# Kernel tuning notes

Hardware: AMD Instinct MI355X
Metric: run time of the kernel (lower is better)

The kernel has to match this reference:

```python
import jax, jax.numpy as jnp
import numpy as np

B, C, H, W = 16, 128, 128, 128
CO = C // 2  # conv output channels


def _binary_activation(x):
    # forward: sign(x); backward: piecewise-polynomial surrogate (STE)
    out_fwd = jnp.sign(x)
    m1 = (x < -1).astype(x.dtype)
    m2 = (x < 0).astype(x.dtype)
    m3 = (x < 1).astype(x.dtype)
    out1 = -1.0 * m1 + (x * x + 2.0 * x) * (1.0 - m1)
    out2 = out1 * m2 + (-x * x + 2.0 * x) * (1.0 - m2)
    out3 = out2 * m3 + 1.0 * (1.0 - m3)
    return jax.lax.stop_gradient(out_fwd) - jax.lax.stop_gradient(out3) + out3


def _binary_weights(conv_w):
    w = conv_w.reshape(CO, C, 3, 3)
    # per-output-channel mean(|w|), detached
    sf = jax.lax.stop_gradient(jnp.mean(jnp.abs(w), axis=(1, 2, 3), keepdims=True))
    bw_ng = sf * jnp.sign(w)
    wc = jnp.clip(w, -1.0, 1.0)
    return jax.lax.stop_gradient(bw_ng) - jax.lax.stop_gradient(wc) + wc


def setup_inputs() -> dict:
    key = jax.random.key(0)
    k1, k2, k3 = jax.random.split(key, 3)
    x = jax.random.normal(k1, (B, C, H, W), dtype=jnp.float32)
    bias1 = jnp.zeros((1, C, 1, 1), dtype=jnp.float32)
    prelu_a = jnp.full((1, C, 1, 1), 0.25, dtype=jnp.float32)
    bias2 = jnp.zeros((1, C, 1, 1), dtype=jnp.float32)
    # stored flat like HardBinaryConv.weights; zero-mean so signs are mixed
    conv_w = jax.random.normal(k2, (CO * C * 9, 1), dtype=jnp.float32) * 0.001
    # grouped 1x1 conv: groups=CO, 2 input channels per group
    pool_w = jax.random.normal(k3, (CO, 2, 1, 1), dtype=jnp.float32) * 0.1
    return {"x": x, "bias1": bias1, "prelu_a": prelu_a, "bias2": bias2,
            "conv_w": conv_w, "pool_w": pool_w}


def reference(x, bias1, prelu_a, bias2, conv_w, pool_w):
    b, c, h, w = x.shape
    co = c // 2
    out = x + bias1
    out = jnp.maximum(out, 0.0) + prelu_a * jnp.minimum(out, 0.0)  # PReLU per-channel
    out = out + bias2
    out = _binary_activation(out)
    bw = _binary_weights(conv_w)
    y = jax.lax.conv_general_dilated(out, bw, window_strides=(1, 1),
                                     padding=((1, 1), (1, 1)),
                                     dimension_numbers=("NCHW", "OIHW", "NCHW"))
    # grouped 1x1 channel pool: out chan o = w[o,0]*x[2o] + w[o,1]*x[2o+1]
    shortcut = jnp.sum(x.reshape(b, co, 2, h, w) * pool_w.reshape(1, co, 2, 1, 1), axis=2)
    y = y + shortcut
    # PixelUnshuffle(2): (B,co,H,W) -> (B,4*co,H/2,W/2)
    ho, wo = h // 2, w // 2
    y = y.reshape(b, co, ho, 2, wo, 2).transpose(0, 1, 3, 5, 2, 4).reshape(b, co * 4, ho, wo)
    return y
```

## Files before the change

### kernel.cpp

```cpp
#include <hip/hip_runtime.h>
#include <stdint.h>

typedef __attribute__((ext_vector_type(4))) float f32x4;
typedef __attribute__((ext_vector_type(4))) unsigned int u32x4;
typedef __attribute__((ext_vector_type(2))) long long i64x2;
typedef long long i64_t;

#define NB 16
#define NC 128
#define NH 128
#define NW 128
#define WP 130

__device__ __forceinline__ int swz7(int wp) { return (wp ^ (wp >> 3)) & 7; }

__global__ __launch_bounds__(256) void k_prep(const float* __restrict__ cw,
                                              const float* __restrict__ b1,
                                              const float* __restrict__ pa,
                                              const float* __restrict__ b2,
                                              float* __restrict__ sf,
                                              float* __restrict__ theta,
                                              unsigned char* __restrict__ wf) {
    int b = blockIdx.x, t = threadIdx.x;
    int f = b * 256 + t;
    int j   = f & 7;
    int kb  = (f >> 11) & 3;
    int p   = f >> 13;
    int l   = (f >> 4) & 63;
    int lg = (l >> 4) & 3;
    int nl  = (f >> 3) & 1;
    int nip = (f >> 10) & 1;
    int o = (nip * 2 + nl) * 16 + (l & 15);
    int c = lg * 16 + (kb & 1) * 8 + (kb >> 1) * 64 + j;
    float wv = cw[o * 1152 + c * 9 + p];
    wf[f] = wv > 0.f ? (unsigned char)0x38
                     : (wv < 0.f ? (unsigned char)0xB8 : (unsigned char)0x00);
    if (b < 64) {
        __shared__ float red[4];
        const float* pp = cw + b * 1152;
        float s = 0.f;
        for (int i = t; i < 1152; i += 256) s += fabsf(pp[i]);
#pragma unroll
        for (int off = 32; off > 0; off >>= 1) s += __shfl_down(s, off);
        if ((t & 63) == 0) red[t >> 6] = s;
        __syncthreads();
        if (t == 0) sf[b] = (red[0] + red[1] + red[2] + red[3]) * (1.0f / 1152.0f);
    }
    if (b == 64 && t < NC) {
        float B1 = b1[t], A = pa[t], B2 = b2[t];
        theta[t] = (-B2 >= 0.f) ? (-B1 - B2) : (-B1 - B2 / A);
    }
}

__device__ __forceinline__ unsigned int pk8(float v, float th) {
    return v > th ? 0x38u : (v < th ? 0xB8u : 0u);
}

__global__ __launch_bounds__(256, 2) void k_fused(
    const float* __restrict__ x, const float* __restrict__ theta,
    const float* __restrict__ pw, const unsigned char* __restrict__ wf,
    const float* __restrict__ sf, float* __restrict__ out) {
    __shared__ __align__(16) unsigned char AT[69632];
    int bxr = blockIdx.x;
    int bx = (bxr & 7) * 128 + (bxr >> 3);
    int nb = bx >> 6;
    int h2b = bx & 63;
    int t = threadIdx.x;
    int wid = t >> 6;
    int l = t & 63;
    int lr = l & 15, lg = l >> 4;

    if (t < 64) {
        int rho = t >> 4, side = (t >> 3) & 1, u = t & 7;
        int wp = side ? (WP - 1) : 0;
        u32x4 z = {0u, 0u, 0u, 0u};
        *(u32x4*)(AT + (size_t)(rho * WP + wp) * NC + ((u ^ swz7(wp)) << 4)) = z;
    }

    int w4 = t & 31, cg = t >> 5;
    const float* xbase = x + ((size_t)nb * NC + cg * 16) * (NH * NW) + 4 * w4;
    f32x4 th0 = *(const f32x4*)(theta + cg * 16);
    f32x4 th1 = *(const f32x4*)(theta + cg * 16 + 4);
    f32x4 th2 = *(const f32x4*)(theta + cg * 16 + 8);
    f32x4 th3 = *(const f32x4*)(theta + cg * 16 + 12);
    f32x4 p0 = *(const f32x4*)(pw + cg * 16);
    f32x4 p1 = *(const f32x4*)(pw + cg * 16 + 4);
    f32x4 p2 = *(const f32x4*)(pw + cg * 16 + 8);
    f32x4 p3 = *(const f32x4*)(pw + cg * 16 + 12);
    float pwv[16] = {p0.x, p0.y, p0.z, p0.w, p1.x, p1.y, p1.z, p1.w,
                     p2.x, p2.y, p2.z, p2.w, p3.x, p3.y, p3.z, p3.w};
    float sc0[8][4], sc1[8][4];

#define LOADX(HH) \
    { const float* xp = xbase + (size_t)(HH) * NW; \
      _Pragma("unroll") for (int cc = 0; cc < 16; ++cc) \
          X[cc] = *(const f32x4*)(xp + (size_t)cc * (NH * NW)); }
#define PACKROW(RHO) \
    _Pragma("unroll") for (int ww = 0; ww < 4; ++ww) { \
        int wp = 4 * w4 + ww + 1; \
        u32x4 v; \
        v.x = pk8(X[0][ww], th0.x) | (pk8(X[1][ww], th0.y) << 8) | \
              (pk8(X[2][ww], th0.z) << 16) | (pk8(X[3][ww], th0.w) << 24); \
        v.y = pk8(X[4][ww], th1.x) | (pk8(X[5][ww], th1.y) << 8) | \
              (pk8(X[6][ww], th1.z) << 16) | (pk8(X[7][ww], th1.w) << 24); \
        v.z = pk8(X[8][ww], th2.x) | (pk8(X[9][ww], th2.y) << 8) | \
              (pk8(X[10][ww], th2.z) << 16) | (pk8(X[11][ww], th2.w) << 24); \
        v.w = pk8(X[12][ww], th3.x) | (pk8(X[13][ww], th3.y) << 8) | \
              (pk8(X[14][ww], th3.z) << 16) | (pk8(X[15][ww], th3.w) << 24); \
        *(u32x4*)(AT + (size_t)((RHO) * WP + wp) * NC + ((cg ^ swz7(wp)) << 4)) = v; \
    }
#define ZEROROW(RHO) \
    { u32x4 z = {0u, 0u, 0u, 0u}; \
      _Pragma("unroll") for (int ww = 0; ww < 4; ++ww) { \
          int wp = 4 * w4 + ww + 1; \
          *(u32x4*)(AT + (size_t)((RHO) * WP + wp) * NC + ((cg ^ swz7(wp)) << 4)) = z; } }
#define SCROW(SC) \
    _Pragma("unroll") for (int i = 0; i < 8; ++i) { \
        float wa = pwv[2 * i], wb = pwv[2 * i + 1]; \
        _Pragma("unroll") for (int ww = 0; ww < 4; ++ww) \
            SC[i][ww] = wa * X[2 * i][ww] + wb * X[2 * i + 1][ww]; \
    }

    if (h2b > 0) {
        f32x4 X[16];
        LOADX(2 * h2b - 1)
        PACKROW(0)
    } else ZEROROW(0)
    {
        f32x4 X[16];
        LOADX(2 * h2b)
        PACKROW(1)
        SCROW(sc0)
    }
    {
        f32x4 X[16];
        LOADX(2 * h2b + 1)
        PACKROW(2)
        SCROW(sc1)
    }
    if (h2b < 63) {
        f32x4 X[16];
        LOADX(2 * h2b + 2)
        PACKROW(3)
    } else ZEROROW(3)

    float sfr[4];
#pragma unroll
    for (int ni = 0; ni < 4; ++ni) sfr[ni] = sf[ni * 16 + lr];

    int w0 = (wid & 1) * 64;
    f32x4 acc[4][4];
    f32x4 zero = {0.f, 0.f, 0.f, 0.f};
#pragma unroll
    for (int mi = 0; mi < 4; ++mi)
#pragma unroll
        for (int ni = 0; ni < 4; ++ni) acc[mi][ni] = zero;
    __syncthreads();

#pragma unroll
    for (int p = 0; p < 9; ++p) {
        int kh = p / 3, kw = p % 3;
        int rho = (wid >> 1) + kh;
        int wp = w0 + kw + lr;
        const unsigned char* ap = AT + (size_t)(rho * WP + wp) * NC;
        const unsigned char* brow = wf + p * 8192 + l * 16;
        i64_t bfr[4][4];
#pragma unroll
        for (int kb = 0; kb < 4; ++kb) {
            i64x2 b01 = *(const i64x2*)(brow + kb * 2048);
            i64x2 b23 = *(const i64x2*)(brow + kb * 2048 + 1024);
            bfr[kb][0] = b01.x; bfr[kb][1] = b01.y;
            bfr[kb][2] = b23.x; bfr[kb][3] = b23.y;
        }
#pragma unroll
        for (int mi = 0; mi < 4; ++mi) {
            int s7m = swz7(wp + mi * 16);
            i64x2 a01 = *(const i64x2*)(ap + mi * 2048 + ((lg ^ s7m) << 4));
            i64x2 a23 = *(const i64x2*)(ap + mi * 2048 + (((lg + 4) ^ s7m) << 4));
            i64_t af[4] = {a01.x, a01.y, a23.x, a23.y};
#pragma unroll
            for (int kb = 0; kb < 4; ++kb)
#pragma unroll
                for (int ni = 0; ni < 4; ++ni)
                    acc[mi][ni] = __builtin_amdgcn_mfma_f32_16x16x32_fp8_fp8(
                        af[kb], bfr[kb][ni], acc[mi][ni], 0, 0, 0);
        }
    }
    __syncthreads();

    float (*Tt)[68] = (float (*)[68])(AT + wid * 17408);
#pragma unroll
    for (int mi = 0; mi < 4; ++mi)
#pragma unroll
        for (int ni = 0; ni < 4; ++ni)
            *(f32x4*)&Tt[ni * 16 + lr][mi * 16 + lg * 4] = acc[mi][ni] * sfr[ni];
    __syncthreads();

    int wha = w4 >> 4, w4l = w4 & 15;
#define EPIROW(R2, SC) { \
    const float (*Ts)[68] = (const float (*)[68])(AT + ((R2) * 2 + wha) * 17408); \
    float* obr = out + (((size_t)nb * 256 + (R2) * 2) * 64 + h2b) * 64 + 2 * w4; \
    _Pragma("unroll") for (int i = 0; i < 8; ++i) { \
        int o = 8 * cg + i; \
        f32x4 cv = *(const f32x4*)&Ts[o][4 * w4l]; \
        float2 A = {cv.x + SC[i][0], cv.z + SC[i][2]}; \
        float2 B = {cv.y + SC[i][1], cv.w + SC[i][3]}; \
        *(float2*)(obr + (size_t)o * 16384)        = A; \
        *(float2*)(obr + (size_t)o * 16384 + 4096) = B; \
    } }
    EPIROW(0, sc0)
    EPIROW(1, sc1)
}

extern "C" void kernel_launch(void* const* d_in, const int* in_sizes, int n_in,
                              void* d_out, int out_size, void* d_ws, size_t ws_size,
                              hipStream_t stream) {
    const float* x  = (const float*)d_in[0];
    const float* b1 = (const float*)d_in[1];
    const float* pa = (const float*)d_in[2];
    const float* b2 = (const float*)d_in[3];
    const float* cw = (const float*)d_in[4];
    const float* pw = (const float*)d_in[5];
    float* out = (float*)d_out;
    float* sf = (float*)d_ws;
    float* theta = (float*)((char*)d_ws + 256);
    unsigned char* wfr = (unsigned char*)d_ws + 768;

    k_prep<<<288, 256, 0, stream>>>(cw, b1, pa, b2, sf, theta, wfr);
    k_fused<<<1024, 256, 0, stream>>>(x, theta, pw, wfr, sf, out);
}
```

Before: 82.52 us.

## Split fused conv tile into column halves to halve LDS and raise occupancy

```diff
diff --git a/kernel.cpp b/kernel.cpp
--- a/kernel.cpp
+++ b/kernel.cpp
@@ -10,7 +10,7 @@
 #define NC 128
 #define NH 128
 #define NW 128
-#define WP 130
+#define WPL 66
 
 __device__ __forceinline__ int swz7(int wp) { return (wp ^ (wp >> 3)) & 7; }
 
@@ -56,91 +56,108 @@
     return v > th ? 0x38u : (v < th ? 0xB8u : 0u);
 }
 
-__global__ __launch_bounds__(256, 2) void k_fused(
+__global__ __launch_bounds__(256, 4) void k_fused(
     const float* __restrict__ x, const float* __restrict__ theta,
     const float* __restrict__ pw, const unsigned char* __restrict__ wf,
     const float* __restrict__ sf, float* __restrict__ out) {
-    __shared__ __align__(16) unsigned char AT[69632];
+    __shared__ __align__(16) unsigned char AT[36864];
     int bxr = blockIdx.x;
-    int bx = (bxr & 7) * 128 + (bxr >> 3);
-    int nb = bx >> 6;
-    int h2b = bx & 63;
+    int bx = (bxr & 7) * 256 + (bxr >> 3);
+    int nb = bx >> 7;
+    int rem = bx & 127;
+    int h2b = rem >> 1;
+    int ch = rem & 1;
     int t = threadIdx.x;
     int wid = t >> 6;
     int l = t & 63;
     int lr = l & 15, lg = l >> 4;
 
     if (t < 64) {
-        int rho = t >> 4, side = (t >> 3) & 1, u = t & 7;
-        int wp = side ? (WP - 1) : 0;
-        u32x4 z = {0u, 0u, 0u, 0u};
-        *(u32x4*)(AT + (size_t)(rho * WP + wp) * NC + ((u ^ swz7(wp)) << 4)) = z;
-    }
-
-    int w4 = t & 31, cg = t >> 5;
-    const float* xbase = x + ((size_t)nb * NC + cg * 16) * (NH * NW) + 4 * w4;
-    f32x4 th0 = *(const f32x4*)(theta + cg * 16);
-    f32x4 th1 = *(const f32x4*)(theta + cg * 16 + 4);
-    f32x4 th2 = *(const f32x4*)(theta + cg * 16 + 8);
-    f32x4 th3 = *(const f32x4*)(theta + cg * 16 + 12);
-    f32x4 p0 = *(const f32x4*)(pw + cg * 16);
-    f32x4 p1 = *(const f32x4*)(pw + cg * 16 + 4);
-    f32x4 p2 = *(const f32x4*)(pw + cg * 16 + 8);
-    f32x4 p3 = *(const f32x4*)(pw + cg * 16 + 12);
-    float pwv[16] = {p0.x, p0.y, p0.z, p0.w, p1.x, p1.y, p1.z, p1.w,
-                     p2.x, p2.y, p2.z, p2.w, p3.x, p3.y, p3.z, p3.w};
-    float sc0[8][4], sc1[8][4];
-
-#define LOADX(HH) \
+        int u = t >> 3;
+        int rho = (t >> 1) & 3;
+        int side = t & 1;
+        int wp = side ? (WPL - 1) : 0;
+        int gpc = 64 * ch + wp;
+        int hh = 2 * h2b + rho - 1;
+        u32x4 v = {0u, 0u, 0u, 0u};
+        if (gpc > 0 && gpc < 129 && hh >= 0 && hh < NH) {
+            const float* xq = x + ((size_t)nb * NC + u * 16) * (NH * NW)
+                                + (size_t)hh * NW + (gpc - 1);
+            float va[16];
+#pragma unroll
+            for (int c = 0; c < 16; ++c) va[c] = xq[(size_t)c * (NH * NW)];
+            f32x4 ta = *(const f32x4*)(theta + u * 16);
+            f32x4 tb = *(const f32x4*)(theta + u * 16 + 4);
+            f32x4 tc = *(const f32x4*)(theta + u * 16 + 8);
+            f32x4 td = *(const f32x4*)(theta + u * 16 + 12);
+            v.x = pk8(va[0], ta.x) | (pk8(va[1], ta.y) << 8) |
+                  (pk8(va[2], ta.z) << 16) | (pk8(va[3], ta.w) << 24);
+            v.y = pk8(va[4], tb.x) | (pk8(va[5], tb.y) << 8) |
+                  (pk8(va[6], tb.z) << 16) | (pk8(va[7], tb.w) << 24);
+            v.z = pk8(va[8], tc.x) | (pk8(va[9], tc.y) << 8) |
+                  (pk8(va[10], tc.z) << 16) | (pk8(va[11], tc.w) << 24);
+            v.w = pk8(va[12], td.x) | (pk8(va[13], td.y) << 8) |
+                  (pk8(va[14], td.z) << 16) | (pk8(va[15], td.w) << 24);
+        }
+        *(u32x4*)(AT + (size_t)(rho * WPL + wp) * NC + ((u ^ swz7(wp)) << 4)) = v;
+    }
+
+    int w4 = t & 15, cg = t >> 4;
+    int uu = cg >> 1, half = cg & 1;
+    const float* xbase = x + ((size_t)nb * NC + cg * 8) * (NH * NW) + 64 * ch + 4 * w4;
+    f32x4 th0 = *(const f32x4*)(theta + cg * 8);
+    f32x4 th1 = *(const f32x4*)(theta + cg * 8 + 4);
+    f32x4 pw0 = *(const f32x4*)(pw + cg * 8);
+    f32x4 pw1 = *(const f32x4*)(pw + cg * 8 + 4);
+    float pwf[8] = {pw0.x, pw0.y, pw0.z, pw0.w, pw1.x, pw1.y, pw1.z, pw1.w};
+    float sc0[4][4], sc1[4][4];
+
+#define LOADX8(HH) \
     { const float* xp = xbase + (size_t)(HH) * NW; \
-      _Pragma("unroll") for (int cc = 0; cc < 16; ++cc) \
+      _Pragma("unroll") for (int cc = 0; cc < 8; ++cc) \
           X[cc] = *(const f32x4*)(xp + (size_t)cc * (NH * NW)); }
 #define PACKROW(RHO) \
     _Pragma("unroll") for (int ww = 0; ww < 4; ++ww) { \
-        int wp = 4 * w4 + ww + 1; \
-        u32x4 v; \
+        int wp = 4 * w4 + 1 + ww; \
+        uint2 v; \
         v.x = pk8(X[0][ww], th0.x) | (pk8(X[1][ww], th0.y) << 8) | \
               (pk8(X[2][ww], th0.z) << 16) | (pk8(X[3][ww], th0.w) << 24); \
         v.y = pk8(X[4][ww], th1.x) | (pk8(X[5][ww], th1.y) << 8) | \
               (pk8(X[6][ww], th1.z) << 16) | (pk8(X[7][ww], th1.w) << 24); \
-        v.z = pk8(X[8][ww], th2.x) | (pk8(X[9][ww], th2.y) << 8) | \
-              (pk8(X[10][ww], th2.z) << 16) | (pk8(X[11][ww], th2.w) << 24); \
-        v.w = pk8(X[12][ww], th3.x) | (pk8(X[13][ww], th3.y) << 8) | \
-              (pk8(X[14][ww], th3.z) << 16) | (pk8(X[15][ww], th3.w) << 24); \
-        *(u32x4*)(AT + (size_t)((RHO) * WP + wp) * NC + ((cg ^ swz7(wp)) << 4)) = v; \
+        *(uint2*)(AT + (size_t)((RHO) * WPL + wp) * NC + ((uu ^ swz7(wp)) << 4) + half * 8) = v; \
     }
 #define ZEROROW(RHO) \
-    { u32x4 z = {0u, 0u, 0u, 0u}; \
+    { uint2 z = {0u, 0u}; \
       _Pragma("unroll") for (int ww = 0; ww < 4; ++ww) { \
-          int wp = 4 * w4 + ww + 1; \
-          *(u32x4*)(AT + (size_t)((RHO) * WP + wp) * NC + ((cg ^ swz7(wp)) << 4)) = z; } }
+          int wp = 4 * w4 + 1 + ww; \
+          *(uint2*)(AT + (size_t)((RHO) * WPL + wp) * NC + ((uu ^ swz7(wp)) << 4) + half * 8) = z; } }
 #define SCROW(SC) \
-    _Pragma("unroll") for (int i = 0; i < 8; ++i) { \
-        float wa = pwv[2 * i], wb = pwv[2 * i + 1]; \
+    _Pragma("unroll") for (int i = 0; i < 4; ++i) { \
+        float wa = pwf[2 * i], wb = pwf[2 * i + 1]; \
         _Pragma("unroll") for (int ww = 0; ww < 4; ++ww) \
             SC[i][ww] = wa * X[2 * i][ww] + wb * X[2 * i + 1][ww]; \
     }
 
     if (h2b > 0) {
-        f32x4 X[16];
-        LOADX(2 * h2b - 1)
+        f32x4 X[8];
+        LOADX8(2 * h2b - 1)
         PACKROW(0)
     } else ZEROROW(0)
     {
-        f32x4 X[16];
-        LOADX(2 * h2b)
+        f32x4 X[8];
+        LOADX8(2 * h2b)
         PACKROW(1)
         SCROW(sc0)
     }
     {
-        f32x4 X[16];
-        LOADX(2 * h2b + 1)
+        f32x4 X[8];
+        LOADX8(2 * h2b + 1)
         PACKROW(2)
         SCROW(sc1)
     }
     if (h2b < 63) {
-        f32x4 X[16];
-        LOADX(2 * h2b + 2)
+        f32x4 X[8];
+        LOADX8(2 * h2b + 2)
         PACKROW(3)
     } else ZEROROW(3)
 
@@ -148,11 +165,11 @@
 #pragma unroll
     for (int ni = 0; ni < 4; ++ni) sfr[ni] = sf[ni * 16 + lr];
 
-    int w0 = (wid & 1) * 64;
-    f32x4 acc[4][4];
+    int w0l = 32 * (wid & 1);
+    f32x4 acc[2][4];
     f32x4 zero = {0.f, 0.f, 0.f, 0.f};
 #pragma unroll
-    for (int mi = 0; mi < 4; ++mi)
+    for (int mi = 0; mi < 2; ++mi)
 #pragma unroll
         for (int ni = 0; ni < 4; ++ni) acc[mi][ni] = zero;
     __syncthreads();
@@ -161,8 +178,8 @@
     for (int p = 0; p < 9; ++p) {
         int kh = p / 3, kw = p % 3;
         int rho = (wid >> 1) + kh;
-        int wp = w0 + kw + lr;
-        const unsigned char* ap = AT + (size_t)(rho * WP + wp) * NC;
+        int wpb = w0l + kw + lr;
+        const unsigned char* ap = AT + (size_t)(rho * WPL + wpb) * NC;
         const unsigned char* brow = wf + p * 8192 + l * 16;
         i64_t bfr[4][4];
 #pragma unroll
@@ -173,8 +190,8 @@
             bfr[kb][2] = b23.x; bfr[kb][3] = b23.y;
         }
 #pragma unroll
-        for (int mi = 0; mi < 4; ++mi) {
-            int s7m = swz7(wp + mi * 16);
+        for (int mi = 0; mi < 2; ++mi) {
+            int s7m = swz7(wpb + mi * 16);
             i64x2 a01 = *(const i64x2*)(ap + mi * 2048 + ((lg ^ s7m) << 4));
             i64x2 a23 = *(const i64x2*)(ap + mi * 2048 + (((lg + 4) ^ s7m) << 4));
             i64_t af[4] = {a01.x, a01.y, a23.x, a23.y};
@@ -188,20 +205,20 @@
     }
     __syncthreads();
 
-    float (*Tt)[68] = (float (*)[68])(AT + wid * 17408);
-#pragma unroll
-    for (int mi = 0; mi < 4; ++mi)
+    float (*Tt)[36] = (float (*)[36])(AT + wid * 9216);
+#pragma unroll
+    for (int mi = 0; mi < 2; ++mi)
 #pragma unroll
         for (int ni = 0; ni < 4; ++ni)
             *(f32x4*)&Tt[ni * 16 + lr][mi * 16 + lg * 4] = acc[mi][ni] * sfr[ni];
     __syncthreads();
 
-    int wha = w4 >> 4, w4l = w4 & 15;
+    int colh_t = w4 >> 3, w4l = w4 & 7;
 #define EPIROW(R2, SC) { \
-    const float (*Ts)[68] = (const float (*)[68])(AT + ((R2) * 2 + wha) * 17408); \
-    float* obr = out + (((size_t)nb * 256 + (R2) * 2) * 64 + h2b) * 64 + 2 * w4; \
-    _Pragma("unroll") for (int i = 0; i < 8; ++i) { \
-        int o = 8 * cg + i; \
+    const float (*Ts)[36] = (const float (*)[36])(AT + ((R2) * 2 + colh_t) * 9216); \
+    float* obr = out + (((size_t)nb * 256 + (R2) * 2) * 64 + h2b) * 64 + 32 * ch + 2 * w4; \
+    _Pragma("unroll") for (int i = 0; i < 4; ++i) { \
+        int o = 4 * cg + i; \
         f32x4 cv = *(const f32x4*)&Ts[o][4 * w4l]; \
         float2 A = {cv.x + SC[i][0], cv.z + SC[i][2]}; \
         float2 B = {cv.y + SC[i][1], cv.w + SC[i][3]}; \
@@ -227,5 +244,5 @@
     unsigned char* wfr = (unsigned char*)d_ws + 768;
 
     k_prep<<<288, 256, 0, stream>>>(cw, b1, pa, b2, sf, theta, wfr);
-    k_fused<<<1024, 256, 0, stream>>>(x, theta, pw, wfr, sf, out);
-}
+    k_fused<<<2048, 256, 0, stream>>>(x, theta, pw, wfr, sf, out);
+}
```

Result: slower. 90.47 us (+9.6%).
